# Kernel optimization log

Hardware: AMD Instinct MI355X
Metric: run time of the kernel (lower is better)

The kernel has to match this reference:

```python
import jax, jax.numpy as jnp
import numpy as np

EPS = 1e-5


def conv2d(x, w, b, stride=1, pad=1):
    out = jax.lax.conv_general_dilated(
        x, w, (stride, stride), [(pad, pad), (pad, pad)],
        dimension_numbers=('NCHW', 'OIHW', 'NCHW'))
    return out + b[None, :, None, None]


def bn_inf(x, gamma, beta, mean, var):
    inv = gamma / jnp.sqrt(var + EPS)
    return x * inv[None, :, None, None] + (beta - mean * inv)[None, :, None, None]


def deform_conv(x, offset, weight, stride, pad, dil):
    # x: [B,Ci,H,W], offset: [B,2*K*K,Ho,Wo] (dy,dx interleaved per kernel pos),
    # weight: [Co,Ci,K,K]. torchvision DeformConv2d v1 semantics, no bias.
    B, Ci, H, W = x.shape
    Co, _, K, _ = weight.shape
    KK = K * K
    Ho = (H + 2 * pad - dil * (K - 1) - 1) // stride + 1
    Wo = (W + 2 * pad - dil * (K - 1) - 1) // stride + 1
    dy = offset[:, 0::2]  # [B,KK,Ho,Wo]
    dx = offset[:, 1::2]
    ky, kx = jnp.meshgrid(jnp.arange(K), jnp.arange(K), indexing='ij')
    ky = ky.reshape(KK).astype(x.dtype)
    kx = kx.reshape(KK).astype(x.dtype)
    base_y = (jnp.arange(Ho) * stride - pad).astype(x.dtype)
    base_x = (jnp.arange(Wo) * stride - pad).astype(x.dtype)
    ys = base_y[None, None, :, None] + (ky * dil)[None, :, None, None] + dy
    xs = base_x[None, None, None, :] + (kx * dil)[None, :, None, None] + dx
    y0 = jnp.floor(ys)
    x0 = jnp.floor(xs)
    fy = ys - y0
    fx = xs - x0

    def gather(img, iy, ix):
        # img: [Ci,H,W]; iy, ix: [KK,Ho,Wo] float integer-valued coords
        valid = (iy >= 0) & (iy < H) & (ix >= 0) & (ix < W)
        iyc = jnp.clip(iy, 0, H - 1).astype(jnp.int32)
        ixc = jnp.clip(ix, 0, W - 1).astype(jnp.int32)
        v = img[:, iyc, ixc]  # [Ci,KK,Ho,Wo]
        return v * valid[None].astype(img.dtype)

    def sample_one(img, y0b, x0b, fyb, fxb):
        w00 = (1 - fyb) * (1 - fxb)
        w01 = (1 - fyb) * fxb
        w10 = fyb * (1 - fxb)
        w11 = fyb * fxb
        s = (gather(img, y0b, x0b) * w00[None]
             + gather(img, y0b, x0b + 1) * w01[None]
             + gather(img, y0b + 1, x0b) * w10[None]
             + gather(img, y0b + 1, x0b + 1) * w11[None])
        return s  # [Ci,KK,Ho,Wo]

    sampled = jax.vmap(sample_one)(x, y0, x0, fy, fx)  # [B,Ci,KK,Ho,Wo]
    return jnp.einsum('oik,bikhw->bohw', weight.reshape(Co, Ci, KK), sampled)


def setup_inputs() -> dict:
    key = jax.random.key(0)
    ks = jax.random.split(key, 16)
    B, C, H, W = 8, 128, 64, 64
    d = dict(
        x=jax.random.normal(ks[0], (B, C, H, W), jnp.float32),
        w_off1=jax.random.normal(ks[1], (18, C, 3, 3), jnp.float32) * 0.01,
        b_off1=jnp.zeros((18,), jnp.float32),
        w_dc1=jax.random.normal(ks[2], (C, C, 3, 3), jnp.float32) * 0.05,
        g1=jnp.ones((C,), jnp.float32),
        beta1=jnp.zeros((C,), jnp.float32),
        m1=jax.random.normal(ks[3], (C,), jnp.float32) * 0.1,
        v1=jax.random.uniform(ks[4], (C,), jnp.float32) + 0.5,
        w_off2=jax.random.normal(ks[5], (18, C, 3, 3), jnp.float32) * 0.01,
        b_off2=jnp.zeros((18,), jnp.float32),
        w_dc2=jax.random.normal(ks[6], (C, C, 3, 3), jnp.float32) * 0.05,
        g2=jnp.ones((C,), jnp.float32),
        beta2=jnp.zeros((C,), jnp.float32),
        m2=jax.random.normal(ks[7], (C,), jnp.float32) * 0.1,
        v2=jax.random.uniform(ks[8], (C,), jnp.float32) + 0.5,
    )
    return d


def reference(x, w_off1, b_off1, w_dc1, g1, beta1, m1, v1,
              w_off2, b_off2, w_dc2, g2, beta2, m2, v2):
    # BasicBlock6 forward (stride=1, in_planes==planes => identity shortcut)
    off1 = conv2d(x, w_off1, b_off1, stride=1, pad=1)
    out = jax.nn.relu(bn_inf(deform_conv(x, off1, w_dc1, 1, 2, 2), g1, beta1, m1, v1))
    off2 = conv2d(out, w_off2, b_off2, stride=1, pad=1)
    out = bn_inf(deform_conv(out, off2, w_dc2, 1, 2, 2), g2, beta2, m2, v2)
    out = out + x  # identity shortcut
    return jax.nn.relu(out)
```

## Files before the change

### kernel.cpp

```cpp
#include <hip/hip_runtime.h>
#include <hip/hip_bf16.h>

#define CH   128
#define HH   64
#define WW   64
#define OFFC 18

typedef __attribute__((ext_vector_type(8))) short bf16x8;
typedef __attribute__((ext_vector_type(4))) short bf16x4;
typedef __attribute__((ext_vector_type(4))) float f32x4;

static __device__ __forceinline__ unsigned short f2bf(float f) {
    __hip_bfloat16 h = __float2bfloat16(f);
    return *reinterpret_cast<unsigned short*>(&h);
}
static __device__ __forceinline__ float bf2f(unsigned short u) {
    union { unsigned int i; float f; } x; x.i = ((unsigned int)u) << 16;
    return x.f;
}

__global__ __launch_bounds__(256) void prep_kernel(
    const float* __restrict__ x, unsigned short* __restrict__ xh,
    const float* __restrict__ wdc1, const float* __restrict__ wdc2,
    const float* __restrict__ wof1, const float* __restrict__ wof2,
    unsigned short* __restrict__ wpk1, unsigned short* __restrict__ wpk2,
    unsigned short* __restrict__ wpo1, unsigned short* __restrict__ wpo2)
{
    __shared__ float s[CH][WW + 1];
    int blk = blockIdx.x;
    int tid = threadIdx.x;

    if (blk < 1152) {
        const float* w = (blk < 576) ? wdc1 : wdc2;
        unsigned short* wp = (blk < 576) ? wpk1 : wpk2;
        int id = (blk % 576) * 256 + tid;
        int j    = id & 7;
        int lane = (id >> 3) & 63;
        int ot   = (id >> 9) & 7;
        int kk   = (id >> 12) & 3;
        int k    = id >> 14;
        int o = ot * 16 + (lane & 15);
        int i = kk * 32 + (lane >> 4) * 8 + j;
        wp[id] = f2bf(w[(o * CH + i) * 9 + k]);
        return;
    }
    if (blk < 1440) {
        const float* w = (blk < 1296) ? wof1 : wof2;
        unsigned short* wp = (blk < 1296) ? wpo1 : wpo2;
        int id = ((blk - 1152) % 144) * 256 + tid;
        int j    = id & 7;
        int lane = (id >> 3) & 63;
        int mt   = (id >> 9) & 1;
        int kk   = (id >> 10) & 3;
        int k    = id >> 12;
        int o = mt * 16 + (lane & 15);
        int i = kk * 32 + (lane >> 4) * 8 + j;
        wp[id] = (o < OFFC) ? f2bf(w[(o * CH + i) * 9 + k]) : (unsigned short)0;
        return;
    }

    int nb = blk - 1440;
    const float* xb = x + ((size_t)(nb >> 6) * CH * HH + (nb & 63)) * WW;

    int c_off = tid >> 4, w0 = (tid & 15) * 4;
    #pragma unroll
    for (int it = 0; it < 8; ++it) {
        int c = it * 16 + c_off;
        float4 vv = *(const float4*)&xb[(size_t)c * HH * WW + w0];
        s[c][w0] = vv.x; s[c][w0 + 1] = vv.y; s[c][w0 + 2] = vv.z; s[c][w0 + 3] = vv.w;
    }
    __syncthreads();

    int w = tid & 63, c0 = (tid >> 6) * 32;
    unsigned short* dst = xh + ((size_t)nb * WW + w) * CH + c0;
    unsigned short tmp[32];
    #pragma unroll
    for (int j = 0; j < 32; ++j) tmp[j] = f2bf(s[c0 + j][w]);
    #pragma unroll
    for (int q = 0; q < 4; ++q)
        *(bf16x8*)(dst + q * 8) = *(const bf16x8*)(tmp + q * 8);
}

__global__ __launch_bounds__(256) void off_conv_mfma_kernel(
    const unsigned short* __restrict__ xh,
    const unsigned short* __restrict__ wpo,
    const float* __restrict__ bias,
    unsigned short* __restrict__ offh)
{
    int wgid = blockIdx.x;
    int blk  = (wgid & 7) * 64 + (wgid >> 3);
    int b = blk >> 6, oh = blk & 63;
    int tid = threadIdx.x;
    int lane = tid & 63;
    int nt = tid >> 6;
    int nl = lane & 15;
    int kg = lane >> 4;

    f32x4 acc0 = {0.f, 0.f, 0.f, 0.f}, acc1 = {0.f, 0.f, 0.f, 0.f};
    const unsigned short* xb = xh + (size_t)b * HH * WW * CH;

    for (int k = 0; k < 9; ++k) {
        int ky = k / 3, kx = k - ky * 3;
        int ih = oh - 1 + ky;
        if (ih < 0 || ih >= HH) continue;
        int iw = nt * 16 + nl + kx - 1;
        bool valid = (iw >= 0) && (iw < WW);
        const unsigned short* row = xb + ((size_t)ih * WW + (valid ? iw : 0)) * CH + kg * 8;
        const unsigned short* wk = wpo + (size_t)k * 4096;
        #pragma unroll
        for (int kk = 0; kk < 4; ++kk) {
            bf16x8 bfrag = {0, 0, 0, 0, 0, 0, 0, 0};
            if (valid) bfrag = *(const bf16x8*)(row + kk * 32);
            bf16x8 a0 = *(const bf16x8*)(wk + (kk * 2 + 0) * 512 + lane * 8);
            bf16x8 a1 = *(const bf16x8*)(wk + (kk * 2 + 1) * 512 + lane * 8);
            acc0 = __builtin_amdgcn_mfma_f32_16x16x32_bf16(a0, bfrag, acc0, 0, 0, 0);
            acc1 = __builtin_amdgcn_mfma_f32_16x16x32_bf16(a1, bfrag, acc1, 0, 0, 0);
        }
    }

    int ow = nt * 16 + nl;
    #pragma unroll
    for (int r = 0; r < 4; ++r) {
        int co = kg * 4 + r;
        offh[(((size_t)b * OFFC + co) * HH + oh) * WW + ow] = f2bf(acc0[r] + bias[co]);
    }
    if (kg == 0) {
        #pragma unroll
        for (int r = 0; r < 2; ++r) {
            int co = 16 + r;
            offh[(((size_t)b * OFFC + co) * HH + oh) * WW + ow] = f2bf(acc1[r] + bias[co]);
        }
    }
}

#define P_COORD(K, OW, CW, PTR) do {                                          \
    int ky_ = (K) / 3, kx_ = (K) - ky_ * 3;                                   \
    float dy_ = off_s[2 * (K)][OW];                                           \
    float dx_ = off_s[2 * (K) + 1][OW];                                       \
    float ys_ = (float)(oh - 2 + ky_ * 2) + dy_;                              \
    float xs_ = (float)((OW) - 2 + kx_ * 2) + dx_;                            \
    float y0f_ = floorf(ys_), x0f_ = floorf(xs_);                             \
    float fy_ = ys_ - y0f_, fx_ = xs_ - x0f_;                                 \
    int y0_ = (int)y0f_, x0_ = (int)x0f_;                                     \
    int y1_ = y0_ + 1, x1_ = x0_ + 1;                                         \
    bool vy0_ = (y0_ >= 0) & (y0_ < HH), vy1_ = (y1_ >= 0) & (y1_ < HH);      \
    bool vx0_ = (x0_ >= 0) & (x0_ < WW), vx1_ = (x1_ >= 0) & (x1_ < WW);      \
    int y0c_ = min(max(y0_, 0), HH - 1), y1c_ = min(max(y1_, 0), HH - 1);     \
    int x0c_ = min(max(x0_, 0), WW - 1), x1c_ = min(max(x1_, 0), WW - 1);     \
    CW[0] = (1.f - fy_) * (1.f - fx_) * ((vy0_ && vx0_) ? 1.f : 0.f);         \
    CW[1] = (1.f - fy_) * fx_         * ((vy0_ && vx1_) ? 1.f : 0.f);         \
    CW[2] = fy_ * (1.f - fx_)         * ((vy1_ && vx0_) ? 1.f : 0.f);         \
    CW[3] = fy_ * fx_                 * ((vy1_ && vx1_) ? 1.f : 0.f);         \
    PTR[0] = xb + ((size_t)(y0c_ * WW + x0c_)) * CH + cig * 8;                \
    PTR[1] = xb + ((size_t)(y0c_ * WW + x1c_)) * CH + cig * 8;                \
    PTR[2] = xb + ((size_t)(y1c_ * WW + x0c_)) * CH + cig * 8;                \
    PTR[3] = xb + ((size_t)(y1c_ * WW + x1c_)) * CH + cig * 8;                \
} while (0)

#define P_ISSUE(PTR, LD) do {                                                 \
    _Pragma("unroll")                                                         \
    for (int c_ = 0; c_ < 4; ++c_) {                                          \
        LD[0][c_] = *(const bf16x8*)(PTR[c_]);                                \
        LD[1][c_] = *(const bf16x8*)(PTR[c_] + 64);                           \
    }                                                                         \
} while (0)

#define P_BLEND(OW, CW, LD, BUF) do {                                         \
    int swz_ = ((OW) & 7) << 4;                                               \
    _Pragma("unroll")                                                         \
    for (int q_ = 0; q_ < 2; ++q_) {                                          \
        union { bf16x8 v8; unsigned short u[8]; } wu_;                        \
        _Pragma("unroll")                                                     \
        for (int j_ = 0; j_ < 8; ++j_) {                                      \
            float val_ = CW[0] * bf2f((unsigned short)LD[q_][0][j_])          \
                       + CW[1] * bf2f((unsigned short)LD[q_][1][j_])          \
                       + CW[2] * bf2f((unsigned short)LD[q_][2][j_])          \
                       + CW[3] * bf2f((unsigned short)LD[q_][3][j_]);         \
            wu_.u[j_] = f2bf(val_);                                           \
        }                                                                     \
        int byte_ = ((OW) * 256 + (q_ * 64 + cig * 8) * 2) ^ swz_;            \
        *(bf16x8*)((char*)sB[BUF] + byte_) = wu_.v8;                          \
    }                                                                         \
} while (0)

#define C_PREF(K, AP) do {                                                    \
    const unsigned short* wk_ = wpk + (size_t)(K) * 16384;                    \
    _Pragma("unroll")                                                         \
    for (int kk_ = 0; kk_ < 4; ++kk_) {                                       \
        AP[kk_ * 2 + 0] = *(const bf16x8*)(wk_ + (size_t)(kk_ * 8 + 2 * cwi)     * 512 + lane * 8); \
        AP[kk_ * 2 + 1] = *(const bf16x8*)(wk_ + (size_t)(kk_ * 8 + 2 * cwi + 1) * 512 + lane * 8); \
    }                                                                         \
} while (0)

__global__ __launch_bounds__(512, 4) void deform_pc_kernel(
    const unsigned short* __restrict__ xh,
    const unsigned short* __restrict__ offh,
    const unsigned short* __restrict__ wpk,
    const float* __restrict__ g, const float* __restrict__ beta,
    const float* __restrict__ m, const float* __restrict__ v,
    const float* __restrict__ residual,
    unsigned short* __restrict__ out_h,
    float* __restrict__ out_f)
{
    __shared__ unsigned short sB[2][64 * 128];
    __shared__ float off_s[OFFC][WW];
    __shared__ int flg[4];

    int wgid = blockIdx.x;
    int blk  = (wgid & 7) * 64 + (wgid >> 3);
    int b = blk >> 6, oh = blk & 63;
    int tid = threadIdx.x, lane = tid & 63, wv = tid >> 6;

    const unsigned short* xb = xh + (size_t)b * HH * WW * CH;

    for (int i = tid; i < OFFC * WW; i += 512) {
        int co = i >> 6, owl = i & 63;
        off_s[co][owl] =
            bf2f(offh[(((size_t)b * OFFC + co) * HH + oh) * WW + owl]);
    }
    if (tid < 4) flg[tid] = 0;
    __syncthreads();

    if (wv < 4) {
        int s_ow = tid >> 3;
        int cig  = tid & 7;

        float cwA[4], cwB[4];
        const unsigned short *ptA[4], *ptB[4];
        bf16x8 ldA[2][4], ldB[2][4];

        P_COORD(0, s_ow, cwA, ptA);
        P_COORD(0, s_ow + 32, cwB, ptB);
        P_ISSUE(ptA, ldA);
        P_ISSUE(ptB, ldB);

        for (int k = 0; k < 9; ++k) {
            int buf = k & 1;
            if (k >= 2) {
                int tgt = 4 * (k >> 1);
                while (__hip_atomic_load(&flg[2 + buf], __ATOMIC_ACQUIRE,
                                         __HIP_MEMORY_SCOPE_WORKGROUP) < tgt)
                    __builtin_amdgcn_s_sleep(1);
            }
            P_BLEND(s_ow,      cwA, ldA, buf);
            P_BLEND(s_ow + 32, cwB, ldB, buf);
            asm volatile("s_waitcnt lgkmcnt(0)" ::: "memory");
            if (lane == 0)
                __hip_atomic_fetch_add(&flg[buf], 1, __ATOMIC_RELEASE,
                                       __HIP_MEMORY_SCOPE_WORKGROUP);
            if (k < 8) {
                P_COORD(k + 1, s_ow, cwA, ptA);
                P_COORD(k + 1, s_ow + 32, cwB, ptB);
                P_ISSUE(ptA, ldA);
                P_ISSUE(ptB, ldB);
            }
        }
    } else {
        int cwi = wv - 4;
        f32x4 acc[2][4];
        #pragma unroll
        for (int a = 0; a < 2; ++a)
            #pragma unroll
            for (int q = 0; q < 4; ++q) acc[a][q] = (f32x4){0.f, 0.f, 0.f, 0.f};

        bf16x8 aP[8];
        C_PREF(0, aP);

        for (int k = 0; k < 9; ++k) {
            int buf = k & 1;
            int tgt = 4 * ((k >> 1) + 1);
            while (__hip_atomic_load(&flg[buf], __ATOMIC_ACQUIRE,
                                     __HIP_MEMORY_SCOPE_WORKGROUP) < tgt)
                __builtin_amdgcn_s_sleep(1);

            __builtin_amdgcn_s_setprio(1);
            #pragma unroll
            for (int kk = 0; kk < 4; ++kk) {
                #pragma unroll
                for (int owt = 0; owt < 4; ++owt) {
                    int owl = owt * 16 + (lane & 15);
                    int rbyte = (owl * 256 + (kk * 32 + (lane >> 4) * 8) * 2)
                                ^ ((owl & 7) << 4);
                    bf16x8 bfv = *(const bf16x8*)((const char*)sB[buf] + rbyte);
                    acc[0][owt] = __builtin_amdgcn_mfma_f32_16x16x32_bf16(
                                      aP[kk * 2 + 0], bfv, acc[0][owt], 0, 0, 0);
                    acc[1][owt] = __builtin_amdgcn_mfma_f32_16x16x32_bf16(
                                      aP[kk * 2 + 1], bfv, acc[1][owt], 0, 0, 0);
                }
            }
            __builtin_amdgcn_s_setprio(0);
            asm volatile("s_waitcnt lgkmcnt(0)" ::: "memory");
            if (lane == 0)
                __hip_atomic_fetch_add(&flg[2 + buf], 1, __ATOMIC_RELEASE,
                                       __HIP_MEMORY_SCOPE_WORKGROUP);
            if (k < 8) C_PREF(k + 1, aP);
        }

        #pragma unroll
        for (int otl = 0; otl < 2; ++otl) {
            int ob = (2 * cwi + otl) * 16 + (lane >> 4) * 4;
            float inv[4], sh[4];
            #pragma unroll
            for (int r = 0; r < 4; ++r) {
                int o = ob + r;
                float iv = g[o] / sqrtf(v[o] + 1e-5f);
                inv[r] = iv; sh[r] = beta[o] - m[o] * iv;
            }
            if (out_h != nullptr) {
                #pragma unroll
                for (int owt = 0; owt < 4; ++owt) {
                    int ow = owt * 16 + (lane & 15);
                    union { bf16x4 v4; unsigned short u[4]; } pk;
                    #pragma unroll
                    for (int r = 0; r < 4; ++r) {
                        float val = acc[otl][owt][r] * inv[r] + sh[r];
                        pk.u[r] = f2bf(fmaxf(val, 0.f));
                    }
                    *(bf16x4*)(out_h + ((size_t)(b * HH + oh) * WW + ow) * CH + ob) = pk.v4;
                }
            } else {
                #pragma unroll
                for (int r = 0; r < 4; ++r) {
                    int o = ob + r;
                    #pragma unroll
                    for (int owt = 0; owt < 4; ++owt) {
                        int ow = owt * 16 + (lane & 15);
                        size_t idx = (((size_t)b * CH + o) * HH + oh) * WW + ow;
                        float val = acc[otl][owt][r] * inv[r] + sh[r] + residual[idx];
                        out_f[idx] = fmaxf(val, 0.f);
                    }
                }
            }
        }
    }
}

extern "C" void kernel_launch(void* const* d_in, const int* in_sizes, int n_in,
                              void* d_out, int out_size, void* d_ws, size_t ws_size,
                              hipStream_t stream)
{
    const float* x      = (const float*)d_in[0];
    const float* w_off1 = (const float*)d_in[1];
    const float* b_off1 = (const float*)d_in[2];
    const float* w_dc1  = (const float*)d_in[3];
    const float* g1     = (const float*)d_in[4];
    const float* beta1  = (const float*)d_in[5];
    const float* m1     = (const float*)d_in[6];
    const float* v1     = (const float*)d_in[7];
    const float* w_off2 = (const float*)d_in[8];
    const float* b_off2 = (const float*)d_in[9];
    const float* w_dc2  = (const float*)d_in[10];
    const float* g2     = (const float*)d_in[11];
    const float* beta2  = (const float*)d_in[12];
    const float* m2     = (const float*)d_in[13];
    const float* v2     = (const float*)d_in[14];
    float* out = (float*)d_out;

    char* ws = (char*)d_ws;
    unsigned short* xh    = (unsigned short*)ws;
    unsigned short* out1h = (unsigned short*)(ws + 8388608);
    unsigned short* offh  = (unsigned short*)(ws + 16777216);
    unsigned short* wpk1  = (unsigned short*)(ws + 17956864);
    unsigned short* wpk2  = (unsigned short*)(ws + 18251776);
    unsigned short* wpo1  = (unsigned short*)(ws + 18546688);
    unsigned short* wpo2  = (unsigned short*)(ws + 18620416);

    prep_kernel<<<1952, 256, 0, stream>>>(x, xh, w_dc1, w_dc2, w_off1, w_off2,
                                          wpk1, wpk2, wpo1, wpo2);

    off_conv_mfma_kernel<<<512, 256, 0, stream>>>(xh, wpo1, b_off1, offh);
    deform_pc_kernel<<<512, 512, 0, stream>>>(xh, offh, wpk1,
                                              g1, beta1, m1, v1,
                                              nullptr, out1h, nullptr);
    off_conv_mfma_kernel<<<512, 256, 0, stream>>>(out1h, wpo2, b_off2, offh);
    deform_pc_kernel<<<512, 512, 0, stream>>>(out1h, offh, wpk2,
                                              g2, beta2, m2, v2,
                                              x, nullptr, out);
}
```

Measured before the change: 90.65 us.

## Fuse offset convolution into deformable conv kernel, computing offsets in LDS

Removes the separate offset-conv kernel and computes the 18-channel offset conv directly inside the deformable conv kernel for each output row. Eight waves split the two 16-row M tiles and four 16-column N tiles, and results go straight to shared memory in fp32. This drops two kernel launches and the bf16 offset buffer round-trip through global memory, and keeps the offsets unrounded. In exchange, each block re-reads three input rows before its main work starts, which lengthens the prologue of the deform kernel.

Result: slower. 98.36 us (+8.5%).

```diff
diff --git a/kernel.cpp b/kernel.cpp
--- a/kernel.cpp
+++ b/kernel.cpp
@@ -79,58 +79,6 @@
     #pragma unroll
     for (int q = 0; q < 4; ++q)
         *(bf16x8*)(dst + q * 8) = *(const bf16x8*)(tmp + q * 8);
-}
-
-__global__ __launch_bounds__(256) void off_conv_mfma_kernel(
-    const unsigned short* __restrict__ xh,
-    const unsigned short* __restrict__ wpo,
-    const float* __restrict__ bias,
-    unsigned short* __restrict__ offh)
-{
-    int wgid = blockIdx.x;
-    int blk  = (wgid & 7) * 64 + (wgid >> 3);
-    int b = blk >> 6, oh = blk & 63;
-    int tid = threadIdx.x;
-    int lane = tid & 63;
-    int nt = tid >> 6;
-    int nl = lane & 15;
-    int kg = lane >> 4;
-
-    f32x4 acc0 = {0.f, 0.f, 0.f, 0.f}, acc1 = {0.f, 0.f, 0.f, 0.f};
-    const unsigned short* xb = xh + (size_t)b * HH * WW * CH;
-
-    for (int k = 0; k < 9; ++k) {
-        int ky = k / 3, kx = k - ky * 3;
-        int ih = oh - 1 + ky;
-        if (ih < 0 || ih >= HH) continue;
-        int iw = nt * 16 + nl + kx - 1;
-        bool valid = (iw >= 0) && (iw < WW);
-        const unsigned short* row = xb + ((size_t)ih * WW + (valid ? iw : 0)) * CH + kg * 8;
-        const unsigned short* wk = wpo + (size_t)k * 4096;
-        #pragma unroll
-        for (int kk = 0; kk < 4; ++kk) {
-            bf16x8 bfrag = {0, 0, 0, 0, 0, 0, 0, 0};
-            if (valid) bfrag = *(const bf16x8*)(row + kk * 32);
-            bf16x8 a0 = *(const bf16x8*)(wk + (kk * 2 + 0) * 512 + lane * 8);
-            bf16x8 a1 = *(const bf16x8*)(wk + (kk * 2 + 1) * 512 + lane * 8);
-            acc0 = __builtin_amdgcn_mfma_f32_16x16x32_bf16(a0, bfrag, acc0, 0, 0, 0);
-            acc1 = __builtin_amdgcn_mfma_f32_16x16x32_bf16(a1, bfrag, acc1, 0, 0, 0);
-        }
-    }
-
-    int ow = nt * 16 + nl;
-    #pragma unroll
-    for (int r = 0; r < 4; ++r) {
-        int co = kg * 4 + r;
-        offh[(((size_t)b * OFFC + co) * HH + oh) * WW + ow] = f2bf(acc0[r] + bias[co]);
-    }
-    if (kg == 0) {
-        #pragma unroll
-        for (int r = 0; r < 2; ++r) {
-            int co = 16 + r;
-            offh[(((size_t)b * OFFC + co) * HH + oh) * WW + ow] = f2bf(acc1[r] + bias[co]);
-        }
-    }
 }
 
 #define P_COORD(K, OW, CW, PTR) do {                                          \
@@ -192,9 +140,10 @@
     }                                                                         \
 } while (0)
 
-__global__ __launch_bounds__(512, 4) void deform_pc_kernel(
-    const unsigned short* __restrict__ xh,
-    const unsigned short* __restrict__ offh,
+__global__ __launch_bounds__(512, 4) void deform_fused_pc_kernel(
+    const unsigned short* __restrict__ xin,
+    const unsigned short* __restrict__ wpo,
+    const float* __restrict__ bias,
     const unsigned short* __restrict__ wpk,
     const float* __restrict__ g, const float* __restrict__ beta,
     const float* __restrict__ m, const float* __restrict__ v,
@@ -211,12 +160,36 @@
     int b = blk >> 6, oh = blk & 63;
     int tid = threadIdx.x, lane = tid & 63, wv = tid >> 6;
 
-    const unsigned short* xb = xh + (size_t)b * HH * WW * CH;
-
-    for (int i = tid; i < OFFC * WW; i += 512) {
-        int co = i >> 6, owl = i & 63;
-        off_s[co][owl] =
-            bf2f(offh[(((size_t)b * OFFC + co) * HH + oh) * WW + owl]);
+    const unsigned short* xb = xin + (size_t)b * HH * WW * CH;
+
+    {
+        int mt = wv >> 2;
+        int nt = wv & 3;
+        int nl = lane & 15, kg = lane >> 4;
+        f32x4 oacc = {0.f, 0.f, 0.f, 0.f};
+        for (int k = 0; k < 9; ++k) {
+            int ky = k / 3, kx = k - ky * 3;
+            int ih = oh - 1 + ky;
+            if (ih < 0 || ih >= HH) continue;
+            int iw = nt * 16 + nl + kx - 1;
+            bool valid = (iw >= 0) && (iw < WW);
+            const unsigned short* row =
+                xb + ((size_t)ih * WW + (valid ? iw : 0)) * CH + kg * 8;
+            const unsigned short* wk = wpo + (size_t)k * 4096;
+            #pragma unroll
+            for (int kk = 0; kk < 4; ++kk) {
+                bf16x8 bfrag = {0, 0, 0, 0, 0, 0, 0, 0};
+                if (valid) bfrag = *(const bf16x8*)(row + kk * 32);
+                bf16x8 a = *(const bf16x8*)(wk + (kk * 2 + mt) * 512 + lane * 8);
+                oacc = __builtin_amdgcn_mfma_f32_16x16x32_bf16(a, bfrag, oacc, 0, 0, 0);
+            }
+        }
+        int ow = nt * 16 + nl;
+        #pragma unroll
+        for (int r = 0; r < 4; ++r) {
+            int co = mt * 16 + kg * 4 + r;
+            if (co < OFFC) off_s[co][ow] = oacc[r] + bias[co];
+        }
     }
     if (tid < 4) flg[tid] = 0;
     __syncthreads();
@@ -359,21 +332,18 @@
     char* ws = (char*)d_ws;
     unsigned short* xh    = (unsigned short*)ws;
     unsigned short* out1h = (unsigned short*)(ws + 8388608);
-    unsigned short* offh  = (unsigned short*)(ws + 16777216);
-    unsigned short* wpk1  = (unsigned short*)(ws + 17956864);
-    unsigned short* wpk2  = (unsigned short*)(ws + 18251776);
-    unsigned short* wpo1  = (unsigned short*)(ws + 18546688);
-    unsigned short* wpo2  = (unsigned short*)(ws + 18620416);
+    unsigned short* wpk1  = (unsigned short*)(ws + 16777216);
+    unsigned short* wpk2  = (unsigned short*)(ws + 17072128);
+    unsigned short* wpo1  = (unsigned short*)(ws + 17367040);
+    unsigned short* wpo2  = (unsigned short*)(ws + 17440768);
 
     prep_kernel<<<1952, 256, 0, stream>>>(x, xh, w_dc1, w_dc2, w_off1, w_off2,
                                           wpk1, wpk2, wpo1, wpo2);
 
-    off_conv_mfma_kernel<<<512, 256, 0, stream>>>(xh, wpo1, b_off1, offh);
-    deform_pc_kernel<<<512, 512, 0, stream>>>(xh, offh, wpk1,
-                                              g1, beta1, m1, v1,
-                                              nullptr, out1h, nullptr);
-    off_conv_mfma_kernel<<<512, 256, 0, stream>>>(out1h, wpo2, b_off2, offh);
-    deform_pc_kernel<<<512, 512, 0, stream>>>(out1h, offh, wpk2,
-                                              g2, beta2, m2, v2,
-                                              x, nullptr, out);
-}
+    deform_fused_pc_kernel<<<512, 512, 0, stream>>>(xh, wpo1, b_off1, wpk1,
+                                                    g1, beta1, m1, v1,
+                                                    nullptr, out1h, nullptr);
+    deform_fused_pc_kernel<<<512, 512, 0, stream>>>(out1h, wpo2, b_off2, wpk2,
+                                                    g2, beta2, m2, v2,
+                                                    x, nullptr, out);
+}
```
